# Kernel tuning notes

Hardware: AMD Instinct MI355X
Metric: run time of the kernel (lower is better)

Reference implementation:

```python
import jax, jax.numpy as jnp
import numpy as np

N_HEADS, D_MODEL, D_HEAD = 16, 1024, 64
BATCH, SEQ = 2, 2048
INIT_STD = 0.02
MASK_FILL = -100000.0  # module uses -1e5, not -inf


def setup_inputs() -> dict:
    key = jax.random.key(0)
    ks = jax.random.split(key, 5)
    x = jax.random.normal(ks[0], (BATCH, SEQ, D_MODEL), dtype=jnp.float32)
    W_Q = INIT_STD * jax.random.normal(ks[1], (N_HEADS, D_MODEL, D_HEAD), dtype=jnp.float32)
    W_K = INIT_STD * jax.random.normal(ks[2], (N_HEADS, D_MODEL, D_HEAD), dtype=jnp.float32)
    W_V = INIT_STD * jax.random.normal(ks[3], (N_HEADS, D_MODEL, D_HEAD), dtype=jnp.float32)
    W_O = INIT_STD * jax.random.normal(ks[4], (N_HEADS, D_HEAD, D_MODEL), dtype=jnp.float32)
    b_Q = jnp.zeros((N_HEADS, D_HEAD), dtype=jnp.float32)
    b_K = jnp.zeros((N_HEADS, D_HEAD), dtype=jnp.float32)
    b_V = jnp.zeros((N_HEADS, D_HEAD), dtype=jnp.float32)
    b_O = jnp.zeros((D_MODEL,), dtype=jnp.float32)
    return {"normalized_resid_pre": x, "W_Q": W_Q, "W_K": W_K, "W_V": W_V,
            "W_O": W_O, "b_Q": b_Q, "b_K": b_K, "b_V": b_V, "b_O": b_O}


def reference(normalized_resid_pre, W_Q, W_K, W_V, W_O, b_Q, b_K, b_V, b_O):
    x = normalized_resid_pre  # [b, s, d_model]
    Q = jnp.einsum('bpd,hde->bphe', x, W_Q) + b_Q  # [b, s, h, dh]
    K = jnp.einsum('bpd,hde->bphe', x, W_K) + b_K
    V = jnp.einsum('bpd,hde->bphe', x, W_V) + b_V
    scale = 1.0 / jnp.sqrt(jnp.float32(D_HEAD))
    scores = jnp.einsum('bqhe,bkhe->bhqk', Q, K) * scale  # [b, h, q, k]
    s = scores.shape[-1]
    causal = jnp.triu(jnp.ones((s, s), dtype=bool), k=1)  # True above diagonal
    scores = jnp.where(causal, jnp.float32(MASK_FILL), scores)
    attn = jax.nn.softmax(scores, axis=-1)
    Z = jnp.einsum('bkhe,bhqk->bqhe', V, attn)  # [b, q, h, dh]
    out = jnp.einsum('bqhe,hed->bqd', Z, W_O) + b_O  # [b, q, d_model]
    return out
```

## Files before the change

kernel.cpp:

```cpp
#include <hip/hip_runtime.h>
#include <math.h>

#define BATCH 2
#define SEQ   2048
#define NH    16
#define DH    64
#define DM    1024

typedef __attribute__((ext_vector_type(8))) short bf16x8;
typedef __attribute__((ext_vector_type(8))) unsigned short u16x8;
typedef __attribute__((ext_vector_type(4))) float f32x4;

__device__ __forceinline__ unsigned short f2bf(float f) {
    union { float f; unsigned u; } v; v.f = f;
    unsigned r = v.u + 0x7FFF + ((v.u >> 16) & 1);
    return (unsigned short)(r >> 16);
}
__device__ __forceinline__ unsigned short f2bf_fast(float f) {
    union { float f; unsigned u; } v; v.f = f;
    return (unsigned short)((v.u + 0x8000u) >> 16);
}

__device__ __forceinline__ void gl2lds16(const void* g, void* l) {
    __builtin_amdgcn_global_load_lds(
        (const __attribute__((address_space(1))) void*)g,
        (__attribute__((address_space(3))) void*)l,
        16, 0, 0);
}

__global__ __launch_bounds__(256) void conv_fused(
    const float* __restrict__ x,
    const float* __restrict__ WQ, const float* __restrict__ WK,
    const float* __restrict__ WV, const float* __restrict__ WO,
    unsigned short* __restrict__ xb,
    unsigned short* __restrict__ Wt, unsigned short* __restrict__ WOt)
{
    __shared__ float sT[64][68];
    const int tid = threadIdx.x;

    if (blockIdx.x < 2048) {
        size_t idx = ((size_t)blockIdx.x * 256 + tid) * 8;
        float4 a = *(const float4*)(x + idx);
        float4 b = *(const float4*)(x + idx + 4);
        u16x8 o;
        o[0] = f2bf(a.x); o[1] = f2bf(a.y); o[2] = f2bf(a.z); o[3] = f2bf(a.w);
        o[4] = f2bf(b.x); o[5] = f2bf(b.y); o[6] = f2bf(b.z); o[7] = f2bf(b.w);
        *(u16x8*)(xb + idx) = o;
        return;
    }
    const int t = blockIdx.x - 2048;
    if (t < 768) {
        int m = t >> 8, rem = t & 255, h = rem >> 4, dblk = rem & 15;
        const float* W = (m == 0) ? WQ : (m == 1) ? WK : WV;
        const float* in = W + (size_t)h * 65536 + dblk * 4096;
#pragma unroll
        for (int it = 0; it < 4; it++) {
            int idx = it * 1024 + tid * 4;
            int r = idx >> 6, c = idx & 63;
            *(float4*)(&sT[r][c]) = *(const float4*)(&in[(size_t)r * 64 + c]);
        }
        __syncthreads();
        unsigned short* out = Wt + (size_t)m * 1048576 + (size_t)h * 65536 + dblk * 64;
#pragma unroll
        for (int it = 0; it < 4; it++) {
            int idx = it * 1024 + tid * 4;
            int e = idx >> 6, d0 = idx & 63;
            ushort4 o;
            unsigned short* op = (unsigned short*)&o;
#pragma unroll
            for (int j = 0; j < 4; j++) op[j] = f2bf(sT[d0 + j][e]);
            *(ushort4*)&out[(size_t)e * 1024 + d0] = o;
        }
    } else {
        int tt = t - 768, rblk = tt >> 4, cblk = tt & 15;
        const float* in = WO + (size_t)rblk * 64 * 1024 + cblk * 64;
#pragma unroll
        for (int it = 0; it < 4; it++) {
            int idx = it * 1024 + tid * 4;
            int r = idx >> 6, c = idx & 63;
            *(float4*)(&sT[r][c]) = *(const float4*)(&in[(size_t)r * 1024 + c]);
        }
        __syncthreads();
        unsigned short* out = WOt + (size_t)cblk * 64 * 1024 + rblk * 64;
#pragma unroll
        for (int it = 0; it < 4; it++) {
            int idx = it * 1024 + tid * 4;
            int d = idx >> 6, he0 = idx & 63;
            ushort4 o;
            unsigned short* op = (unsigned short*)&o;
#pragma unroll
            for (int j = 0; j < 4; j++) op[j] = f2bf(sT[he0 + j][d]);
            *(ushort4*)&out[(size_t)d * 1024 + he0] = o;
        }
    }
}

__global__ __launch_bounds__(256) void qkv_mfma(
    const unsigned short* __restrict__ xb,
    const unsigned short* __restrict__ Wt,
    const float* __restrict__ bQ, const float* __restrict__ bK,
    const float* __restrict__ bV,
    unsigned short* __restrict__ Q, unsigned short* __restrict__ K,
    unsigned short* __restrict__ Vt)
{
    __shared__ __align__(16) unsigned short sA[2][128 * 64];
    __shared__ __align__(16) unsigned short sB[2][128 * 64];

    const int rowTile = blockIdx.x;
    const int m  = blockIdx.y >> 3;
    const int hp = blockIdx.y & 7;
    const unsigned short* Wm = Wt + (size_t)m * 1048576 + (size_t)hp * 2 * 65536;

    const int tid  = threadIdx.x;
    const int w    = tid >> 6;
    const int lane = tid & 63;
    const int l15  = lane & 15;
    const int quad = lane >> 4;
    const int rw   = (w & 1) * 64;
    const int cw   = (w >> 1) * 64;
    const int rowBase = rowTile * 128;

    const int crow = lane >> 3;
    const int ccs  = (((lane & 7) ^ crow) * 8);

    f32x4 acc[4][4];
#pragma unroll
    for (int i = 0; i < 4; i++)
#pragma unroll
        for (int j = 0; j < 4; j++) acc[i][j] = (f32x4){0.f, 0.f, 0.f, 0.f};

#pragma unroll
    for (int c = 0; c < 4; c++) {
        const int chunk = w * 4 + c;
        const int rr = chunk * 8 + crow;
        gl2lds16(&xb[(size_t)(rowBase + rr) * DM + ccs], &sA[0][chunk * 512]);
        gl2lds16(&Wm[(size_t)rr * DM + ccs],             &sB[0][chunk * 512]);
    }

    for (int kt = 0; kt < 16; kt++) {
        __syncthreads();
        if (kt < 15) {
            const int k1 = (kt + 1) * 64;
            unsigned short* dA = sA[(kt + 1) & 1];
            unsigned short* dB = sB[(kt + 1) & 1];
#pragma unroll
            for (int c = 0; c < 4; c++) {
                const int chunk = w * 4 + c;
                const int rr = chunk * 8 + crow;
                gl2lds16(&xb[(size_t)(rowBase + rr) * DM + k1 + ccs], &dA[chunk * 512]);
                gl2lds16(&Wm[(size_t)rr * DM + k1 + ccs],             &dB[chunk * 512]);
            }
        }
        const unsigned short* pA = sA[kt & 1];
        const unsigned short* pB = sB[kt & 1];

#pragma unroll
        for (int ks = 0; ks < 2; ks++) {
            bf16x8 af[4], bf[4];
#pragma unroll
            for (int i = 0; i < 4; i++) {
                int ar = rw + i * 16 + l15;
                af[i] = *(const bf16x8*)&pA[ar * 64 + (((ks * 4 + quad) ^ (ar & 7)) * 8)];
            }
#pragma unroll
            for (int j = 0; j < 4; j++) {
                int br = cw + j * 16 + l15;
                bf[j] = *(const bf16x8*)&pB[br * 64 + (((ks * 4 + quad) ^ (br & 7)) * 8)];
            }
            if (m == 2) {
#pragma unroll
                for (int i = 0; i < 4; i++)
#pragma unroll
                    for (int j = 0; j < 4; j++)
                        acc[i][j] = __builtin_amdgcn_mfma_f32_16x16x32_bf16(
                            af[i], bf[j], acc[i][j], 0, 0, 0);
            } else {
#pragma unroll
                for (int i = 0; i < 4; i++)
#pragma unroll
                    for (int j = 0; j < 4; j++)
                        acc[i][j] = __builtin_amdgcn_mfma_f32_16x16x32_bf16(
                            bf[j], af[i], acc[i][j], 0, 0, 0);
            }
        }
    }

    if (m == 2) {
#pragma unroll
        for (int j = 0; j < 4; j++) {
            int col = cw + j * 16 + l15;
            int h = hp * 2 + (col >> 6);
            int e = col & 63;
            float bv = bV[h * DH + e];
#pragma unroll
            for (int i = 0; i < 4; i++) {
                int row0 = rowBase + rw + i * 16 + quad * 4;
                int b = row0 >> 11, s0 = row0 & 2047;
                ushort4 o;
                unsigned short* op = (unsigned short*)&o;
#pragma unroll
                for (int r = 0; r < 4; r++) op[r] = f2bf(acc[i][j][r] + bv);
                *(ushort4*)&Vt[(((size_t)b * NH + h) * DH + e) * SEQ + s0] = o;
            }
        }
    } else {
        const float* bias = (m == 0) ? bQ : bK;
        unsigned short* Out = (m == 0) ? Q : K;
        const float scale = (m == 0) ? 0.125f : 1.0f;
        float4 bb[4];
        int hj[4], e0j[4];
#pragma unroll
        for (int j = 0; j < 4; j++) {
            int col0 = cw + j * 16 + quad * 4;
            hj[j] = hp * 2 + (col0 >> 6);
            e0j[j] = col0 & 63;
            bb[j] = *(const float4*)&bias[hj[j] * DH + e0j[j]];
        }
#pragma unroll
        for (int i = 0; i < 4; i++) {
            int row = rowBase + rw + i * 16 + l15;
            int b = row >> 11, s = row & 2047;
#pragma unroll
            for (int j = 0; j < 4; j++) {
                const float* bp = (const float*)&bb[j];
                ushort4 o;
                unsigned short* op = (unsigned short*)&o;
#pragma unroll
                for (int r = 0; r < 4; r++)
                    op[r] = f2bf((acc[i][j][r] + bp[r]) * scale);
                *(ushort4*)&Out[(((size_t)b * NH + hj[j]) * SEQ + s) * DH + e0j[j]] = o;
            }
        }
    }
}

__global__ __launch_bounds__(256) void attn_mfma(
    const unsigned short* __restrict__ Q,
    const unsigned short* __restrict__ K,
    const unsigned short* __restrict__ Vt,
    unsigned short* __restrict__ Z)
{
    __shared__ __align__(16) unsigned short sK [2][64 * 64];
    __shared__ __align__(16) unsigned short sV [2][64 * 64];
    __shared__ __align__(16) unsigned short sPA[64 * 72];
    __shared__ __align__(16) unsigned short sPB[64 * 72];

    const int h   = blockIdx.x & 15;
    const int b   = (blockIdx.x >> 4) & 1;
    const int i   = blockIdx.x >> 5;
    const int qtA = i;
    const int qtB = 31 - i;

    const int tid  = threadIdx.x;
    const int w    = tid >> 6;
    const int lane = tid & 63;
    const int l15  = lane & 15;
    const int quad = lane >> 4;

    const size_t headOff = ((size_t)b * NH + h) * SEQ * DH;
    const unsigned short* Qh  = Q  + headOff;
    const unsigned short* Kh  = K  + headOff;
    const unsigned short* Vth = Vt + headOff;

    const unsigned short* qrowA =
        Qh + (size_t)(qtA * 64 + w * 16 + l15) * DH + quad * 8;
    const unsigned short* qrowB =
        Qh + (size_t)(qtB * 64 + w * 16 + l15) * DH + quad * 8;
    bf16x8 qA[2], qB[2];
    qA[0] = *(const bf16x8*)(qrowA);  qA[1] = *(const bf16x8*)(qrowA + 32);
    qB[0] = *(const bf16x8*)(qrowB);  qB[1] = *(const bf16x8*)(qrowB + 32);

    f32x4 OA[4], OB[4];
#pragma unroll
    for (int s = 0; s < 4; s++) {
        OA[s] = (f32x4){0.f, 0.f, 0.f, 0.f};
        OB[s] = (f32x4){0.f, 0.f, 0.f, 0.f};
    }
    float lAa = 0.f, lBa = 0.f;

    const int crow = lane >> 3;
    const int ccs  = (((lane & 7) ^ crow) * 8);

#pragma unroll
    for (int c = 0; c < 2; c++) {
        const int chunk = w * 2 + c;
        const int rr = chunk * 8 + crow;
        gl2lds16(&Kh[(size_t)rr * DH + ccs],  &sK[0][chunk * 512]);
        gl2lds16(&Vth[(size_t)rr * SEQ + ccs], &sV[0][chunk * 512]);
    }

    for (int kt = 0; kt <= qtB; kt++) {
        __syncthreads();
        if (kt < qtB) {
            const int k1 = (kt + 1) * 64;
            unsigned short* dK = sK[(kt + 1) & 1];
            unsigned short* dV = sV[(kt + 1) & 1];
#pragma unroll
            for (int c = 0; c < 2; c++) {
                const int chunk = w * 2 + c;
                const int rr = chunk * 8 + crow;
                gl2lds16(&Kh[(size_t)(k1 + rr) * DH + ccs], &dK[chunk * 512]);
                gl2lds16(&Vth[(size_t)rr * SEQ + k1 + ccs], &dV[chunk * 512]);
            }
        }
        const unsigned short* pK = sK[kt & 1];
        const unsigned short* pV = sV[kt & 1];

        bf16x8 kf[8], vf[8];
#pragma unroll
        for (int ks = 0; ks < 2; ks++)
#pragma unroll
            for (int sub = 0; sub < 4; sub++) {
                int rr = sub * 16 + l15;
                int sw = ((ks * 4 + quad) ^ (rr & 7)) * 8;
                kf[ks * 4 + sub] = *(const bf16x8*)&pK[rr * 64 + sw];
                vf[ks * 4 + sub] = *(const bf16x8*)&pV[rr * 64 + sw];
            }

        const bool doA = (kt <= qtA);

        f32x4 SB[4];
#pragma unroll
        for (int s = 0; s < 4; s++) SB[s] = (f32x4){0.f, 0.f, 0.f, 0.f};
#pragma unroll
        for (int ks = 0; ks < 2; ks++)
#pragma unroll
            for (int sub = 0; sub < 4; sub++)
                SB[sub] = __builtin_amdgcn_mfma_f32_16x16x32_bf16(
                    kf[ks * 4 + sub], qB[ks], SB[sub], 0, 0, 0);
        f32x4 SA[4];
        if (doA) {
#pragma unroll
            for (int s = 0; s < 4; s++) SA[s] = (f32x4){0.f, 0.f, 0.f, 0.f};
#pragma unroll
            for (int ks = 0; ks < 2; ks++)
#pragma unroll
                for (int sub = 0; sub < 4; sub++)
                    SA[sub] = __builtin_amdgcn_mfma_f32_16x16x32_bf16(
                        kf[ks * 4 + sub], qA[ks], SA[sub], 0, 0, 0);
        }

        const bool diagB = (kt == qtB);
#pragma unroll
        for (int sub = 0; sub < 4; sub++) {
            ushort4 o;
            unsigned short* op = (unsigned short*)&o;
#pragma unroll
            for (int r = 0; r < 4; r++) {
                float pb = __expf(SB[sub][r]);
                if (diagB && (sub * 16 + quad * 4 + r > w * 16 + l15)) pb = 0.f;
                lBa += pb;
                op[r] = f2bf_fast(pb);
            }
            *(ushort4*)&sPB[(w * 16 + l15) * 72 + sub * 16 + quad * 4] = o;
        }
        if (doA) {
            const bool diagA = (kt == qtA);
#pragma unroll
            for (int sub = 0; sub < 4; sub++) {
                ushort4 o;
                unsigned short* op = (unsigned short*)&o;
#pragma unroll
                for (int r = 0; r < 4; r++) {
                    float pa = __expf(SA[sub][r]);
                    if (diagA && (sub * 16 + quad * 4 + r > w * 16 + l15)) pa = 0.f;
                    lAa += pa;
                    op[r] = f2bf_fast(pa);
                }
                *(ushort4*)&sPA[(w * 16 + l15) * 72 + sub * 16 + quad * 4] = o;
            }
        }
        __builtin_amdgcn_wave_barrier();

#pragma unroll
        for (int ks = 0; ks < 2; ks++) {
            bf16x8 pb = *(const bf16x8*)
                &sPB[(w * 16 + l15) * 72 + ks * 32 + quad * 8];
#pragma unroll
            for (int sub = 0; sub < 4; sub++)
                OB[sub] = __builtin_amdgcn_mfma_f32_16x16x32_bf16(
                    vf[ks * 4 + sub], pb, OB[sub], 0, 0, 0);
        }
        if (doA) {
#pragma unroll
            for (int ks = 0; ks < 2; ks++) {
                bf16x8 pa = *(const bf16x8*)
                    &sPA[(w * 16 + l15) * 72 + ks * 32 + quad * 8];
#pragma unroll
                for (int sub = 0; sub < 4; sub++)
                    OA[sub] = __builtin_amdgcn_mfma_f32_16x16x32_bf16(
                        vf[ks * 4 + sub], pa, OA[sub], 0, 0, 0);
            }
        }
        __builtin_amdgcn_wave_barrier();
    }

    lAa += __shfl_xor(lAa, 16, 64);
    lAa += __shfl_xor(lAa, 32, 64);
    lBa += __shfl_xor(lBa, 16, 64);
    lBa += __shfl_xor(lBa, 32, 64);
    const float rlA = 1.0f / lAa;
    const float rlB = 1.0f / lBa;

#pragma unroll
    for (int half = 0; half < 2; half++) {
        const int qt = half ? qtB : qtA;
        const f32x4* O4 = half ? OB : OA;
        const float rl = half ? rlB : rlA;
        const int q = qt * 64 + w * 16 + l15;
        unsigned short* zrow = Z + ((size_t)b * SEQ + q) * DM + h * DH;
#pragma unroll
        for (int sub = 0; sub < 4; sub++) {
            ushort4 o;
            unsigned short* op = (unsigned short*)&o;
#pragma unroll
            for (int r = 0; r < 4; r++) op[r] = f2bf(O4[sub][r] * rl);
            *(ushort4*)&zrow[sub * 16 + quad * 4] = o;
        }
    }
}

__global__ __launch_bounds__(256) void out_mfma(
    const unsigned short* __restrict__ Zb,
    const unsigned short* __restrict__ WOt,
    const float* __restrict__ bO,
    float* __restrict__ out)
{
    __shared__ __align__(16) unsigned short sA[2][64 * 64];
    __shared__ __align__(16) unsigned short sB[2][128 * 64];

    const int rowTile = blockIdx.x;
    const int colTile = blockIdx.y;
    const int rowBase = rowTile * 64;
    const int colBase = colTile * 128;

    const int tid  = threadIdx.x;
    const int w    = tid >> 6;
    const int lane = tid & 63;
    const int l15  = lane & 15;
    const int quad = lane >> 4;
    const int rw   = (w & 1) * 32;
    const int cw   = (w >> 1) * 64;

    const int crow = lane >> 3;
    const int ccs  = (((lane & 7) ^ crow) * 8);

    f32x4 acc[2][4];
#pragma unroll
    for (int i = 0; i < 2; i++)
#pragma unroll
        for (int j = 0; j < 4; j++) acc[i][j] = (f32x4){0.f, 0.f, 0.f, 0.f};

#pragma unroll
    for (int c = 0; c < 2; c++) {
        const int chunk = w * 2 + c;
        const int rr = chunk * 8 + crow;
        gl2lds16(&Zb[(size_t)(rowBase + rr) * DM + ccs], &sA[0][chunk * 512]);
    }
#pragma unroll
    for (int c = 0; c < 4; c++) {
        const int chunk = w * 4 + c;
        const int rr = chunk * 8 + crow;
        gl2lds16(&WOt[(size_t)(colBase + rr) * DM + ccs], &sB[0][chunk * 512]);
    }

    for (int kt = 0; kt < 16; kt++) {
        __syncthreads();
        if (kt < 15) {
            const int k1 = (kt + 1) * 64;
            unsigned short* dA = sA[(kt + 1) & 1];
            unsigned short* dB = sB[(kt + 1) & 1];
#pragma unroll
            for (int c = 0; c < 2; c++) {
                const int chunk = w * 2 + c;
                const int rr = chunk * 8 + crow;
                gl2lds16(&Zb[(size_t)(rowBase + rr) * DM + k1 + ccs], &dA[chunk * 512]);
            }
#pragma unroll
            for (int c = 0; c < 4; c++) {
                const int chunk = w * 4 + c;
                const int rr = chunk * 8 + crow;
                gl2lds16(&WOt[(size_t)(colBase + rr) * DM + k1 + ccs], &dB[chunk * 512]);
            }
        }
        const unsigned short* pA = sA[kt & 1];
        const unsigned short* pB = sB[kt & 1];

#pragma unroll
        for (int ks = 0; ks < 2; ks++) {
            bf16x8 af[2], bf[4];
#pragma unroll
            for (int i = 0; i < 2; i++) {
                int ar = rw + i * 16 + l15;
                af[i] = *(const bf16x8*)&pA[ar * 64 + (((ks * 4 + quad) ^ (ar & 7)) * 8)];
            }
#pragma unroll
            for (int j = 0; j < 4; j++) {
                int br = cw + j * 16 + l15;
                bf[j] = *(const bf16x8*)&pB[br * 64 + (((ks * 4 + quad) ^ (br & 7)) * 8)];
            }
#pragma unroll
            for (int i = 0; i < 2; i++)
#pragma unroll
                for (int j = 0; j < 4; j++)
                    acc[i][j] = __builtin_amdgcn_mfma_f32_16x16x32_bf16(
                        bf[j], af[i], acc[i][j], 0, 0, 0);
        }
    }

#pragma unroll
    for (int i = 0; i < 2; i++) {
        int row = rowBase + rw + i * 16 + l15;
#pragma unroll
        for (int j = 0; j < 4; j++) {
            int col0 = colBase + cw + j * 16 + quad * 4;
            float4 o;
            o.x = acc[i][j][0] + bO[col0 + 0];
            o.y = acc[i][j][1] + bO[col0 + 1];
            o.z = acc[i][j][2] + bO[col0 + 2];
            o.w = acc[i][j][3] + bO[col0 + 3];
            *(float4*)&out[(size_t)row * DM + col0] = o;
        }
    }
}

extern "C" void kernel_launch(void* const* d_in, const int* in_sizes, int n_in,
                              void* d_out, int out_size, void* d_ws, size_t ws_size,
                              hipStream_t stream)
{
    const float* x  = (const float*)d_in[0];
    const float* WQ = (const float*)d_in[1];
    const float* WK = (const float*)d_in[2];
    const float* WV = (const float*)d_in[3];
    const float* WO = (const float*)d_in[4];
    const float* bQ = (const float*)d_in[5];
    const float* bK = (const float*)d_in[6];
    const float* bV = (const float*)d_in[7];
    const float* bO = (const float*)d_in[8];
    float* out = (float*)d_out;

    const size_t M4 = 4194304;
    unsigned short* xb  = (unsigned short*)d_ws;
    unsigned short* Wt  = xb + M4;
    unsigned short* WOt = Wt + 3 * 1048576;
    unsigned short* Qw  = WOt + 1048576;
    unsigned short* Kw  = Qw + M4;
    unsigned short* Vtw = Kw + M4;
    unsigned short* Zb  = xb;

    conv_fused<<<3072, 256, 0, stream>>>(x, WQ, WK, WV, WO, xb, Wt, WOt);

    dim3 g1(32, 24);
    qkv_mfma<<<g1, 256, 0, stream>>>(xb, Wt, bQ, bK, bV, Qw, Kw, Vtw);

    attn_mfma<<<512, 256, 0, stream>>>(Qw, Kw, Vtw, Zb);

    dim3 g3(64, 8);
    out_mfma<<<g3, 256, 0, stream>>>(Zb, WOt, bO, out);
}
```

Before: 183.8 us.

## Single-buffer A tile via register prefetch and raise QKV occupancy hint

The QKV projection GEMM now loads the next x tile into registers instead of asynchronously into a second LDS buffer. After an extra barrier it writes them into a single shared A buffer, while W keeps double-buffered global-to-LDS loads. This cuts LDS use by 16 KB per block, and the launch bounds add a minimum of 3 blocks per SIMD to raise occupancy. The cost is an extra barrier per k-step, more register pressure under the tighter bound, and exposed LDS write latency.

```diff
diff --git a/kernel.cpp b/kernel.cpp
--- a/kernel.cpp
+++ b/kernel.cpp
@@ -95,7 +95,7 @@
     }
 }
 
-__global__ __launch_bounds__(256) void qkv_mfma(
+__global__ __launch_bounds__(256, 3) void qkv_mfma(
     const unsigned short* __restrict__ xb,
     const unsigned short* __restrict__ Wt,
     const float* __restrict__ bQ, const float* __restrict__ bK,
@@ -103,7 +103,7 @@
     unsigned short* __restrict__ Q, unsigned short* __restrict__ K,
     unsigned short* __restrict__ Vt)
 {
-    __shared__ __align__(16) unsigned short sA[2][128 * 64];
+    __shared__ __align__(16) unsigned short sA[128 * 64];
     __shared__ __align__(16) unsigned short sB[2][128 * 64];
 
     const int rowTile = blockIdx.x;
@@ -129,29 +129,48 @@
 #pragma unroll
         for (int j = 0; j < 4; j++) acc[i][j] = (f32x4){0.f, 0.f, 0.f, 0.f};
 
-#pragma unroll
-    for (int c = 0; c < 4; c++) {
-        const int chunk = w * 4 + c;
-        const int rr = chunk * 8 + crow;
-        gl2lds16(&xb[(size_t)(rowBase + rr) * DM + ccs], &sA[0][chunk * 512]);
-        gl2lds16(&Wm[(size_t)rr * DM + ccs],             &sB[0][chunk * 512]);
+    {
+        u16x8 a0[4];
+#pragma unroll
+        for (int c = 0; c < 4; c++) {
+            const int chunk = w * 4 + c;
+            const int rr = chunk * 8 + crow;
+            a0[c] = *(const u16x8*)&xb[(size_t)(rowBase + rr) * DM + ccs];
+        }
+#pragma unroll
+        for (int c = 0; c < 4; c++) {
+            const int chunk = w * 4 + c;
+            const int rr = chunk * 8 + crow;
+            gl2lds16(&Wm[(size_t)rr * DM + ccs], &sB[0][chunk * 512]);
+        }
+#pragma unroll
+        for (int c = 0; c < 4; c++) {
+            const int chunk = w * 4 + c;
+            *(u16x8*)&sA[chunk * 512 + lane * 8] = a0[c];
+        }
     }
 
     for (int kt = 0; kt < 16; kt++) {
         __syncthreads();
+
+        u16x8 aN[4];
         if (kt < 15) {
             const int k1 = (kt + 1) * 64;
-            unsigned short* dA = sA[(kt + 1) & 1];
-            unsigned short* dB = sB[(kt + 1) & 1];
 #pragma unroll
             for (int c = 0; c < 4; c++) {
                 const int chunk = w * 4 + c;
                 const int rr = chunk * 8 + crow;
-                gl2lds16(&xb[(size_t)(rowBase + rr) * DM + k1 + ccs], &dA[chunk * 512]);
-                gl2lds16(&Wm[(size_t)rr * DM + k1 + ccs],             &dB[chunk * 512]);
-            }
-        }
-        const unsigned short* pA = sA[kt & 1];
+                aN[c] = *(const u16x8*)&xb[(size_t)(rowBase + rr) * DM + k1 + ccs];
+            }
+            unsigned short* dB = sB[(kt + 1) & 1];
+#pragma unroll
+            for (int c = 0; c < 4; c++) {
+                const int chunk = w * 4 + c;
+                const int rr = chunk * 8 + crow;
+                gl2lds16(&Wm[(size_t)rr * DM + k1 + ccs], &dB[chunk * 512]);
+            }
+        }
+
         const unsigned short* pB = sB[kt & 1];
 
 #pragma unroll
@@ -160,7 +179,7 @@
 #pragma unroll
             for (int i = 0; i < 4; i++) {
                 int ar = rw + i * 16 + l15;
-                af[i] = *(const bf16x8*)&pA[ar * 64 + (((ks * 4 + quad) ^ (ar & 7)) * 8)];
+                af[i] = *(const bf16x8*)&sA[ar * 64 + (((ks * 4 + quad) ^ (ar & 7)) * 8)];
             }
 #pragma unroll
             for (int j = 0; j < 4; j++) {
@@ -181,6 +200,17 @@
                     for (int j = 0; j < 4; j++)
                         acc[i][j] = __builtin_amdgcn_mfma_f32_16x16x32_bf16(
                             bf[j], af[i], acc[i][j], 0, 0, 0);
+            }
+        }
+
+        if (kt < 15) {
+            __builtin_amdgcn_sched_barrier(0);
+            __builtin_amdgcn_s_barrier();
+            __builtin_amdgcn_sched_barrier(0);
+#pragma unroll
+            for (int c = 0; c < 4; c++) {
+                const int chunk = w * 4 + c;
+                *(u16x8*)&sA[chunk * 512 + lane * 8] = aN[c];
             }
         }
     }
```

New measurement: 250.8 us. +36.5%, slower.

## Split paired attention query tiles into one tile per block, use exp2

Applied to the files above, without the earlier changes.

Each attention block previously handled two query tiles (i and 31-i) to balance the causal work. Now it handles one tile, and twice as many blocks are launched, scheduled longest-first so the heaviest tiles start earliest. This trades the paired balancing for more parallelism and lower register and LDS use per block. The Q scale now folds in log2(e) so the kernel can call exp2 directly instead of __expf, and the P buffer in LDS switches from padding to an XOR swizzle.

```diff
diff --git a/kernel.cpp b/kernel.cpp
--- a/kernel.cpp
+++ b/kernel.cpp
@@ -27,6 +27,8 @@
         (__attribute__((address_space(3))) void*)l,
         16, 0, 0);
 }
+
+#define QSCALE 0.18033688011112042f
 
 __global__ __launch_bounds__(256) void conv_fused(
     const float* __restrict__ x,
@@ -206,7 +208,7 @@
     } else {
         const float* bias = (m == 0) ? bQ : bK;
         unsigned short* Out = (m == 0) ? Q : K;
-        const float scale = (m == 0) ? 0.125f : 1.0f;
+        const float scale = (m == 0) ? QSCALE : 1.0f;
         float4 bb[4];
         int hj[4], e0j[4];
 #pragma unroll
@@ -240,43 +242,35 @@
     const unsigned short* __restrict__ Vt,
     unsigned short* __restrict__ Z)
 {
-    __shared__ __align__(16) unsigned short sK [2][64 * 64];
-    __shared__ __align__(16) unsigned short sV [2][64 * 64];
-    __shared__ __align__(16) unsigned short sPA[64 * 72];
-    __shared__ __align__(16) unsigned short sPB[64 * 72];
-
-    const int h   = blockIdx.x & 15;
-    const int b   = (blockIdx.x >> 4) & 1;
-    const int i   = blockIdx.x >> 5;
-    const int qtA = i;
-    const int qtB = 31 - i;
+    __shared__ __align__(16) unsigned short sK[2][64 * 64];
+    __shared__ __align__(16) unsigned short sV[2][64 * 64];
+    __shared__ __align__(16) unsigned short sP[64 * 64];
+
+    const int h  = blockIdx.x & 15;
+    const int b  = (blockIdx.x >> 4) & 1;
+    const int qt = 31 - (blockIdx.x >> 5);
 
     const int tid  = threadIdx.x;
     const int w    = tid >> 6;
     const int lane = tid & 63;
     const int l15  = lane & 15;
     const int quad = lane >> 4;
+    const int row  = w * 16 + l15;
 
     const size_t headOff = ((size_t)b * NH + h) * SEQ * DH;
     const unsigned short* Qh  = Q  + headOff;
     const unsigned short* Kh  = K  + headOff;
     const unsigned short* Vth = Vt + headOff;
 
-    const unsigned short* qrowA =
-        Qh + (size_t)(qtA * 64 + w * 16 + l15) * DH + quad * 8;
-    const unsigned short* qrowB =
-        Qh + (size_t)(qtB * 64 + w * 16 + l15) * DH + quad * 8;
-    bf16x8 qA[2], qB[2];
-    qA[0] = *(const bf16x8*)(qrowA);  qA[1] = *(const bf16x8*)(qrowA + 32);
-    qB[0] = *(const bf16x8*)(qrowB);  qB[1] = *(const bf16x8*)(qrowB + 32);
-
-    f32x4 OA[4], OB[4];
-#pragma unroll
-    for (int s = 0; s < 4; s++) {
-        OA[s] = (f32x4){0.f, 0.f, 0.f, 0.f};
-        OB[s] = (f32x4){0.f, 0.f, 0.f, 0.f};
-    }
-    float lAa = 0.f, lBa = 0.f;
+    const unsigned short* qrow =
+        Qh + (size_t)(qt * 64 + row) * DH + quad * 8;
+    bf16x8 q0 = *(const bf16x8*)(qrow);
+    bf16x8 q1 = *(const bf16x8*)(qrow + 32);
+
+    f32x4 O[4];
+#pragma unroll
+    for (int s = 0; s < 4; s++) O[s] = (f32x4){0.f, 0.f, 0.f, 0.f};
+    float la = 0.f;
 
     const int crow = lane >> 3;
     const int ccs  = (((lane & 7) ^ crow) * 8);
@@ -285,13 +279,16 @@
     for (int c = 0; c < 2; c++) {
         const int chunk = w * 2 + c;
         const int rr = chunk * 8 + crow;
-        gl2lds16(&Kh[(size_t)rr * DH + ccs],  &sK[0][chunk * 512]);
+        gl2lds16(&Kh[(size_t)rr * DH + ccs],   &sK[0][chunk * 512]);
         gl2lds16(&Vth[(size_t)rr * SEQ + ccs], &sV[0][chunk * 512]);
     }
 
-    for (int kt = 0; kt <= qtB; kt++) {
+    const int pwBase = row * 64 + (quad & 1) * 4;
+    const int prBase = row * 64;
+
+    for (int kt = 0; kt <= qt; kt++) {
         __syncthreads();
-        if (kt < qtB) {
+        if (kt < qt) {
             const int k1 = (kt + 1) * 64;
             unsigned short* dK = sK[(kt + 1) & 1];
             unsigned short* dV = sV[(kt + 1) & 1];
@@ -317,104 +314,60 @@
                 vf[ks * 4 + sub] = *(const bf16x8*)&pV[rr * 64 + sw];
             }
 
-        const bool doA = (kt <= qtA);
-
-        f32x4 SB[4];
-#pragma unroll
-        for (int s = 0; s < 4; s++) SB[s] = (f32x4){0.f, 0.f, 0.f, 0.f};
-#pragma unroll
-        for (int ks = 0; ks < 2; ks++)
-#pragma unroll
-            for (int sub = 0; sub < 4; sub++)
-                SB[sub] = __builtin_amdgcn_mfma_f32_16x16x32_bf16(
-                    kf[ks * 4 + sub], qB[ks], SB[sub], 0, 0, 0);
-        f32x4 SA[4];
-        if (doA) {
-#pragma unroll
-            for (int s = 0; s < 4; s++) SA[s] = (f32x4){0.f, 0.f, 0.f, 0.f};
-#pragma unroll
-            for (int ks = 0; ks < 2; ks++)
-#pragma unroll
-                for (int sub = 0; sub < 4; sub++)
-                    SA[sub] = __builtin_amdgcn_mfma_f32_16x16x32_bf16(
-                        kf[ks * 4 + sub], qA[ks], SA[sub], 0, 0, 0);
-        }
-
-        const bool diagB = (kt == qtB);
+        f32x4 S4[4];
+#pragma unroll
+        for (int s = 0; s < 4; s++) S4[s] = (f32x4){0.f, 0.f, 0.f, 0.f};
+#pragma unroll
+        for (int sub = 0; sub < 4; sub++)
+            S4[sub] = __builtin_amdgcn_mfma_f32_16x16x32_bf16(
+                kf[sub], q0, S4[sub], 0, 0, 0);
+#pragma unroll
+        for (int sub = 0; sub < 4; sub++)
+            S4[sub] = __builtin_amdgcn_mfma_f32_16x16x32_bf16(
+                kf[4 + sub], q1, S4[sub], 0, 0, 0);
+
+        const bool diag = (kt == qt);
 #pragma unroll
         for (int sub = 0; sub < 4; sub++) {
             ushort4 o;
             unsigned short* op = (unsigned short*)&o;
 #pragma unroll
             for (int r = 0; r < 4; r++) {
-                float pb = __expf(SB[sub][r]);
-                if (diagB && (sub * 16 + quad * 4 + r > w * 16 + l15)) pb = 0.f;
-                lBa += pb;
-                op[r] = f2bf_fast(pb);
-            }
-            *(ushort4*)&sPB[(w * 16 + l15) * 72 + sub * 16 + quad * 4] = o;
-        }
-        if (doA) {
-            const bool diagA = (kt == qtA);
-#pragma unroll
-            for (int sub = 0; sub < 4; sub++) {
-                ushort4 o;
-                unsigned short* op = (unsigned short*)&o;
-#pragma unroll
-                for (int r = 0; r < 4; r++) {
-                    float pa = __expf(SA[sub][r]);
-                    if (diagA && (sub * 16 + quad * 4 + r > w * 16 + l15)) pa = 0.f;
-                    lAa += pa;
-                    op[r] = f2bf_fast(pa);
-                }
-                *(ushort4*)&sPA[(w * 16 + l15) * 72 + sub * 16 + quad * 4] = o;
-            }
+                float p = __builtin_exp2f(S4[sub][r]);
+                if (diag && (sub * 16 + quad * 4 + r > row)) p = 0.f;
+                la += p;
+                op[r] = f2bf_fast(p);
+            }
+            int chunk = sub * 2 + (quad >> 1);
+            *(ushort4*)&sP[pwBase + ((chunk ^ (row & 7)) * 8)] = o;
         }
         __builtin_amdgcn_wave_barrier();
 
 #pragma unroll
         for (int ks = 0; ks < 2; ks++) {
             bf16x8 pb = *(const bf16x8*)
-                &sPB[(w * 16 + l15) * 72 + ks * 32 + quad * 8];
+                &sP[prBase + (((ks * 4 + quad) ^ (row & 7)) * 8)];
 #pragma unroll
             for (int sub = 0; sub < 4; sub++)
-                OB[sub] = __builtin_amdgcn_mfma_f32_16x16x32_bf16(
-                    vf[ks * 4 + sub], pb, OB[sub], 0, 0, 0);
-        }
-        if (doA) {
-#pragma unroll
-            for (int ks = 0; ks < 2; ks++) {
-                bf16x8 pa = *(const bf16x8*)
-                    &sPA[(w * 16 + l15) * 72 + ks * 32 + quad * 8];
-#pragma unroll
-                for (int sub = 0; sub < 4; sub++)
-                    OA[sub] = __builtin_amdgcn_mfma_f32_16x16x32_bf16(
-                        vf[ks * 4 + sub], pa, OA[sub], 0, 0, 0);
-            }
+                O[sub] = __builtin_amdgcn_mfma_f32_16x16x32_bf16(
+                    vf[ks * 4 + sub], pb, O[sub], 0, 0, 0);
         }
         __builtin_amdgcn_wave_barrier();
     }
 
-    lAa += __shfl_xor(lAa, 16, 64);
-    lAa += __shfl_xor(lAa, 32, 64);
-    lBa += __shfl_xor(lBa, 16, 64);
-    lBa += __shfl_xor(lBa, 32, 64);
-    const float rlA = 1.0f / lAa;
-    const float rlB = 1.0f / lBa;
-
-#pragma unroll
-    for (int half = 0; half < 2; half++) {
-        const int qt = half ? qtB : qtA;
-        const f32x4* O4 = half ? OB : OA;
-        const float rl = half ? rlB : rlA;
-        const int q = qt * 64 + w * 16 + l15;
+    la += __shfl_xor(la, 16, 64);
+    la += __shfl_xor(la, 32, 64);
+    const float rl = 1.0f / la;
+
+    {
+        const int q = qt * 64 + row;
         unsigned short* zrow = Z + ((size_t)b * SEQ + q) * DM + h * DH;
 #pragma unroll
         for (int sub = 0; sub < 4; sub++) {
             ushort4 o;
             unsigned short* op = (unsigned short*)&o;
 #pragma unroll
-            for (int r = 0; r < 4; r++) op[r] = f2bf(O4[sub][r] * rl);
+            for (int r = 0; r < 4; r++) op[r] = f2bf(O[sub][r] * rl);
             *(ushort4*)&zrow[sub * 16 + quad * 4] = o;
         }
     }
@@ -553,7 +506,7 @@
     dim3 g1(32, 24);
     qkv_mfma<<<g1, 256, 0, stream>>>(xb, Wt, bQ, bK, bV, Qw, Kw, Vtw);
 
-    attn_mfma<<<512, 256, 0, stream>>>(Qw, Kw, Vtw, Zb);
+    attn_mfma<<<1024, 256, 0, stream>>>(Qw, Kw, Vtw, Zb);
 
     dim3 g3(64, 8);
     out_mfma<<<g3, 256, 0, stream>>>(Zb, WOt, bO, out);
```

Measured after the change: 186.1 us. No clear change (+1.3%).
